# Kernel tuning notes

Measured on AMD Instinct MI355X. Metric: run time of the kernel, lower is better.

The kernel has to match this reference:

```python
import jax, jax.numpy as jnp
import numpy as np

K = 1024  # eval-mode k = min(int(2**20 / 4 / 256), H*W=25200) = 1024


def setup_inputs() -> dict:
    key = jax.random.key(0)
    k1, k2, k3 = jax.random.split(key, 3)
    B, L, C, H, W = 4, 5, 256, 100, 252
    Cp = 2  # anchor_nums
    x = jax.random.normal(k1, (B, L, C, H, W), dtype=jnp.float32)
    psm = jax.random.normal(k2, (B, L, Cp, H, W), dtype=jnp.float32)
    mask = jax.random.randint(k3, (B, L), 0, 2, dtype=jnp.int32)
    return {"x": x, "psm": psm, "mask": mask}


def reference(x, psm, mask):
    # x: [B,L,C,H,W]; psm: [B,L,Cp,H,W]; mask: [B,L]
    B, L, C, H, W = x.shape
    ego = psm[:, :1]                                  # [B,1,Cp,H,W]
    # residual psm -> sigmoid -> max over psm channel dim (dim=0 per pair)
    fmap = jnp.max(jax.nn.sigmoid(psm - ego), axis=2)  # [B,L,H,W]
    flat = fmap.reshape(B, L, H * W)
    topv = jax.lax.top_k(flat, K)[0]                   # sorted descending
    thresh = topv[..., K - 1]                          # min of top-k == k-th largest, [B,L]
    fmask = (flat >= thresh[..., None]).astype(x.dtype).reshape(B, L, 1, H, W)
    keep = (mask != 0)[:, :, None, None, None]         # [B,L,1,1,1]
    l_is_ego = (jnp.arange(L) == 0)[None, :, None, None, None]
    # l==0 -> passthrough; mask==0 -> zeros; else x * filter_mask
    out = jnp.where(l_is_ego, x, jnp.where(keep, x * fmask, jnp.zeros((), x.dtype)))
    return out
```

## Files before the change

kernel.cpp:

```cpp
#include <hip/hip_runtime.h>

#define BB 4
#define LL 5
#define CC 256
#define HH 100
#define WW 252
#define HW (HH * WW)
#define HW4 (HW / 4)
#define NPAIR (BB * LL)
#define KSEL 1024

#define OG 4
#define OBLK 256
#define OSPAN (OBLK * OG)
#define NXBLK ((HW4 + OSPAN - 1) / OSPAN)

typedef float vf4 __attribute__((ext_vector_type(4)));

__device__ __forceinline__ float stable_sigmoid(float d) {
    if (d >= 0.0f) {
        return 1.0f / (1.0f + expf(-d));
    } else {
        float e = expf(d);
        return e / (1.0f + e);
    }
}

__global__ __launch_bounds__(256) void sig_kernel(const float* __restrict__ psm,
                                                  float* __restrict__ s) {
    int i = blockIdx.x * 256 + threadIdx.x;
    if (i >= NPAIR * HW4) return;
    int hw4 = i % HW4;
    int bl  = i / HW4;
    int b   = bl / LL;
    const vf4* p  = (const vf4*)(psm + (size_t)bl * 2 * HW);
    const vf4* pe = (const vf4*)(psm + (size_t)(b * LL) * 2 * HW);
    vf4 a0 = p[hw4];
    vf4 a1 = p[HW4 + hw4];
    vf4 e0 = pe[hw4];
    vf4 e1 = pe[HW4 + hw4];
    vf4 r;
    r.x = stable_sigmoid(fmaxf(a0.x - e0.x, a1.x - e1.x));
    r.y = stable_sigmoid(fmaxf(a0.y - e0.y, a1.y - e1.y));
    r.z = stable_sigmoid(fmaxf(a0.z - e0.z, a1.z - e1.z));
    r.w = stable_sigmoid(fmaxf(a0.w - e0.w, a1.w - e1.w));
    ((vf4*)s)[i] = r;
}

__global__ __launch_bounds__(1024) void select_kernel(const float* __restrict__ s,
                                                      const int* __restrict__ mask,
                                                      float* __restrict__ thresh) {
    int bl = blockIdx.x;
    int l  = bl % LL;
    if (l == 0 || mask[bl] == 0) {
        if (threadIdx.x == 0) thresh[bl] = __int_as_float(0x7f800000);
        return;
    }
    const float* base = s + (size_t)bl * HW;
    __shared__ unsigned hist[256];
    __shared__ unsigned sh_prefix;
    __shared__ int sh_k;
    if (threadIdx.x == 0) { sh_prefix = 0u; sh_k = KSEL; }
    __syncthreads();

    const int HWR = ((HW + 1023) / 1024) * 1024;

    for (int sh = 24; sh >= 0; sh -= 8) {
        if (threadIdx.x < 256) hist[threadIdx.x] = 0u;
        __syncthreads();
        unsigned prefix = sh_prefix;
        for (int i = threadIdx.x; i < HWR; i += 1024) {
            bool valid = (i < HW);
            unsigned u = valid ? __float_as_uint(base[i]) : 0u;
            bool ok = valid && ((sh == 24) || (((u ^ prefix) >> (sh + 8)) == 0u));
            unsigned d = (u >> sh) & 255u;
            unsigned long long act = __ballot(ok);
            if (ok) {
                unsigned long long m = act;
                #pragma unroll
                for (int b = 0; b < 8; ++b) {
                    unsigned long long bm = __ballot((d >> b) & 1u);
                    m &= ((d >> b) & 1u) ? bm : ~bm;
                }
                int lane = threadIdx.x & 63;
                int leader = __ffsll((unsigned long long)m) - 1;
                if (lane == leader)
                    atomicAdd(&hist[d], (unsigned)__popcll(m));
            }
        }
        __syncthreads();
        if (threadIdx.x == 0) {
            int kk = sh_k;
            int bin = 255;
            for (; bin > 0; --bin) {
                int c = (int)hist[bin];
                if (kk - c <= 0) break;
                kk -= c;
            }
            sh_prefix = prefix | ((unsigned)bin << sh);
            sh_k = kk;
        }
        __syncthreads();
    }
    if (threadIdx.x == 0) thresh[bl] = __uint_as_float(sh_prefix);
}

__global__ __launch_bounds__(256) void pack_kernel(const float* __restrict__ s,
                                                   const int* __restrict__ mask,
                                                   const float* __restrict__ thresh,
                                                   unsigned char* __restrict__ pmask) {
    int bl = blockIdx.y;
    int l  = bl % LL;
    if (l == 0 || mask[bl] == 0) return;
    int hw4 = blockIdx.x * 256 + threadIdx.x;
    if (hw4 >= HW4) return;
    float t = thresh[bl];
    vf4 sv = ((const vf4*)s)[bl * HW4 + hw4];
    unsigned m = (sv.x >= t ? 1u : 0u) | (sv.y >= t ? 2u : 0u)
               | (sv.z >= t ? 4u : 0u) | (sv.w >= t ? 8u : 0u);
    pmask[bl * HW4 + hw4] = (unsigned char)m;
}

__global__ __launch_bounds__(256) void out_kernel(const float* __restrict__ x,
                                                  const int* __restrict__ mask,
                                                  const unsigned char* __restrict__ pmask,
                                                  float* __restrict__ out) {
    int bl = blockIdx.z;
    int c  = blockIdx.y;
    int l  = bl % LL;
    int hw4_0 = blockIdx.x * OSPAN + (int)threadIdx.x;
    size_t cbase = ((size_t)(bl * CC + c)) * HW4;
    const vf4* x4 = (const vf4*)x;
    vf4* o4 = (vf4*)out;

    if (l == 0) {
        #pragma unroll
        for (int j = 0; j < OG; ++j) {
            int hw4 = hw4_0 + j * OBLK;
            if (hw4 < HW4) {
                vf4 v = __builtin_nontemporal_load(&x4[cbase + hw4]);
                __builtin_nontemporal_store(v, &o4[cbase + hw4]);
            }
        }
        return;
    }
    if (mask[bl] == 0) {
        vf4 z = (vf4)(0.f);
        #pragma unroll
        for (int j = 0; j < OG; ++j) {
            int hw4 = hw4_0 + j * OBLK;
            if (hw4 < HW4) __builtin_nontemporal_store(z, &o4[cbase + hw4]);
        }
        return;
    }

    const unsigned char* pm = pmask + bl * HW4;
    #pragma unroll
    for (int j = 0; j < OG; ++j) {
        int hw4 = hw4_0 + j * OBLK;
        if (hw4 >= HW4) continue;
        unsigned m = pm[hw4];
        vf4 res = (vf4)(0.f);
        if (m) {
            vf4 xv = __builtin_nontemporal_load(&x4[cbase + hw4]);
            res.x = (m & 1u) ? xv.x : 0.f;
            res.y = (m & 2u) ? xv.y : 0.f;
            res.z = (m & 4u) ? xv.z : 0.f;
            res.w = (m & 8u) ? xv.w : 0.f;
        }
        __builtin_nontemporal_store(res, &o4[cbase + hw4]);
    }
}

extern "C" void kernel_launch(void* const* d_in, const int* in_sizes, int n_in,
                              void* d_out, int out_size, void* d_ws, size_t ws_size,
                              hipStream_t stream) {
    const float* x   = (const float*)d_in[0];
    const float* psm = (const float*)d_in[1];
    const int* mask  = (const int*)d_in[2];
    float* out = (float*)d_out;

    float* s      = (float*)d_ws;
    float* thresh = s + (size_t)NPAIR * HW;
    unsigned char* pmask = (unsigned char*)(thresh + NPAIR);

    int n_s4 = NPAIR * HW4;
    sig_kernel<<<(n_s4 + 255) / 256, 256, 0, stream>>>(psm, s);
    select_kernel<<<NPAIR, 1024, 0, stream>>>(s, mask, thresh);

    dim3 gp((HW4 + 255) / 256, NPAIR);
    pack_kernel<<<gp, 256, 0, stream>>>(s, mask, thresh, pmask);

    dim3 grid(NXBLK, CC, NPAIR);
    out_kernel<<<grid, 256, 0, stream>>>(x, mask, pmask, out);
}
```

Measured before the change: 834.2 us.

## Fuse sigmoid, radix select and mask packing into one LDS-resident kernel

Three kernels (sigmoid map, per-pair radix select, mask packing) are merged into one kernel that launches one 1024-thread block per non-ego pair. The full sigmoid map for a pair is kept in a large static LDS array (about 100 KB), so the global scratch write and re-reads are gone. The threshold buffer and two launches are also removed. In exchange, the heavy LDS use limits each CU to one such block, and the front end now runs on only 16 blocks.

```diff
diff --git a/kernel.cpp b/kernel.cpp
--- a/kernel.cpp
+++ b/kernel.cpp
@@ -26,64 +26,57 @@
     }
 }
 
-__global__ __launch_bounds__(256) void sig_kernel(const float* __restrict__ psm,
-                                                  float* __restrict__ s) {
-    int i = blockIdx.x * 256 + threadIdx.x;
-    if (i >= NPAIR * HW4) return;
-    int hw4 = i % HW4;
-    int bl  = i / HW4;
-    int b   = bl / LL;
-    const vf4* p  = (const vf4*)(psm + (size_t)bl * 2 * HW);
-    const vf4* pe = (const vf4*)(psm + (size_t)(b * LL) * 2 * HW);
-    vf4 a0 = p[hw4];
-    vf4 a1 = p[HW4 + hw4];
-    vf4 e0 = pe[hw4];
-    vf4 e1 = pe[HW4 + hw4];
-    vf4 r;
-    r.x = stable_sigmoid(fmaxf(a0.x - e0.x, a1.x - e1.x));
-    r.y = stable_sigmoid(fmaxf(a0.y - e0.y, a1.y - e1.y));
-    r.z = stable_sigmoid(fmaxf(a0.z - e0.z, a1.z - e1.z));
-    r.w = stable_sigmoid(fmaxf(a0.w - e0.w, a1.w - e1.w));
-    ((vf4*)s)[i] = r;
-}
+__global__ __launch_bounds__(1024) void fused_select_pack(
+        const float* __restrict__ psm,
+        const int* __restrict__ mask,
+        unsigned char* __restrict__ pmask) {
+    int idx = blockIdx.x;
+    int b   = idx / (LL - 1);
+    int l   = 1 + idx % (LL - 1);
+    int bl  = b * LL + l;
+    if (mask[bl] == 0) return;
 
-__global__ __launch_bounds__(1024) void select_kernel(const float* __restrict__ s,
-                                                      const int* __restrict__ mask,
-                                                      float* __restrict__ thresh) {
-    int bl = blockIdx.x;
-    int l  = bl % LL;
-    if (l == 0 || mask[bl] == 0) {
-        if (threadIdx.x == 0) thresh[bl] = __int_as_float(0x7f800000);
-        return;
-    }
-    const float* base = s + (size_t)bl * HW;
+    __shared__ float s_lds[HW];
     __shared__ unsigned hist[256];
     __shared__ unsigned sh_prefix;
     __shared__ int sh_k;
+
+    const vf4* p  = (const vf4*)(psm + (size_t)bl * 2 * HW);
+    const vf4* pe = (const vf4*)(psm + (size_t)(b * LL) * 2 * HW);
+    for (int i = threadIdx.x; i < HW4; i += 1024) {
+        vf4 a0 = p[i];
+        vf4 a1 = p[HW4 + i];
+        vf4 e0 = pe[i];
+        vf4 e1 = pe[HW4 + i];
+        vf4 r;
+        r.x = stable_sigmoid(fmaxf(a0.x - e0.x, a1.x - e1.x));
+        r.y = stable_sigmoid(fmaxf(a0.y - e0.y, a1.y - e1.y));
+        r.z = stable_sigmoid(fmaxf(a0.z - e0.z, a1.z - e1.z));
+        r.w = stable_sigmoid(fmaxf(a0.w - e0.w, a1.w - e1.w));
+        ((vf4*)s_lds)[i] = r;
+    }
     if (threadIdx.x == 0) { sh_prefix = 0u; sh_k = KSEL; }
     __syncthreads();
 
     const int HWR = ((HW + 1023) / 1024) * 1024;
-
     for (int sh = 24; sh >= 0; sh -= 8) {
         if (threadIdx.x < 256) hist[threadIdx.x] = 0u;
         __syncthreads();
         unsigned prefix = sh_prefix;
         for (int i = threadIdx.x; i < HWR; i += 1024) {
             bool valid = (i < HW);
-            unsigned u = valid ? __float_as_uint(base[i]) : 0u;
+            unsigned u = valid ? __float_as_uint(s_lds[i]) : 0u;
             bool ok = valid && ((sh == 24) || (((u ^ prefix) >> (sh + 8)) == 0u));
             unsigned d = (u >> sh) & 255u;
-            unsigned long long act = __ballot(ok);
             if (ok) {
-                unsigned long long m = act;
+                unsigned long long m = __ballot(ok);
                 #pragma unroll
-                for (int b = 0; b < 8; ++b) {
-                    unsigned long long bm = __ballot((d >> b) & 1u);
-                    m &= ((d >> b) & 1u) ? bm : ~bm;
+                for (int bit = 0; bit < 8; ++bit) {
+                    unsigned long long bm = __ballot((d >> bit) & 1u);
+                    m &= ((d >> bit) & 1u) ? bm : ~bm;
                 }
                 int lane = threadIdx.x & 63;
-                int leader = __ffsll((unsigned long long)m) - 1;
+                int leader = __ffsll(m) - 1;
                 if (lane == leader)
                     atomicAdd(&hist[d], (unsigned)__popcll(m));
             }
@@ -102,23 +95,15 @@
         }
         __syncthreads();
     }
-    if (threadIdx.x == 0) thresh[bl] = __uint_as_float(sh_prefix);
-}
+    float t = __uint_as_float(sh_prefix);
 
-__global__ __launch_bounds__(256) void pack_kernel(const float* __restrict__ s,
-                                                   const int* __restrict__ mask,
-                                                   const float* __restrict__ thresh,
-                                                   unsigned char* __restrict__ pmask) {
-    int bl = blockIdx.y;
-    int l  = bl % LL;
-    if (l == 0 || mask[bl] == 0) return;
-    int hw4 = blockIdx.x * 256 + threadIdx.x;
-    if (hw4 >= HW4) return;
-    float t = thresh[bl];
-    vf4 sv = ((const vf4*)s)[bl * HW4 + hw4];
-    unsigned m = (sv.x >= t ? 1u : 0u) | (sv.y >= t ? 2u : 0u)
-               | (sv.z >= t ? 4u : 0u) | (sv.w >= t ? 8u : 0u);
-    pmask[bl * HW4 + hw4] = (unsigned char)m;
+    unsigned char* pm = pmask + bl * HW4;
+    for (int i = threadIdx.x; i < HW4; i += 1024) {
+        vf4 sv = ((const vf4*)s_lds)[i];
+        unsigned m = (sv.x >= t ? 1u : 0u) | (sv.y >= t ? 2u : 0u)
+                   | (sv.z >= t ? 4u : 0u) | (sv.w >= t ? 8u : 0u);
+        pm[i] = (unsigned char)m;
+    }
 }
 
 __global__ __launch_bounds__(256) void out_kernel(const float* __restrict__ x,
@@ -180,16 +165,9 @@
     const int* mask  = (const int*)d_in[2];
     float* out = (float*)d_out;
 
-    float* s      = (float*)d_ws;
-    float* thresh = s + (size_t)NPAIR * HW;
-    unsigned char* pmask = (unsigned char*)(thresh + NPAIR);
+    unsigned char* pmask = (unsigned char*)d_ws;
 
-    int n_s4 = NPAIR * HW4;
-    sig_kernel<<<(n_s4 + 255) / 256, 256, 0, stream>>>(psm, s);
-    select_kernel<<<NPAIR, 1024, 0, stream>>>(s, mask, thresh);
-
-    dim3 gp((HW4 + 255) / 256, NPAIR);
-    pack_kernel<<<gp, 256, 0, stream>>>(s, mask, thresh, pmask);
+    fused_select_pack<<<BB * (LL - 1), 1024, 0, stream>>>(psm, mask, pmask);
 
     dim3 grid(NXBLK, CC, NPAIR);
     out_kernel<<<grid, 256, 0, stream>>>(x, mask, pmask, out);
```

Result: no change. 833.7 us (-0.1%).
